# Performance work log

Hardware: AMD Instinct MI355X
Metric: run time of the kernel (lower is better)

Reference implementation:

```python
import jax, jax.numpy as jnp
import numpy as np

S, M, V, E, H = 128, 256, 32000, 1024, 512
PAD_ID = V - 1  # pad_id=-1 normalized to vocab-1


def setup_inputs() -> dict:
    key = jax.random.key(0)
    ks = jax.random.split(key, 9)
    F_lens = jax.random.randint(ks[0], (M,), 1, S + 1)
    tok = jax.random.randint(ks[1], (S, M), 1, PAD_ID)  # avoid 0 and PAD for valid tokens
    valid = jnp.arange(S)[:, None] < F_lens[None, :]
    F = jnp.where(valid, tok, PAD_ID)
    sc = 1.0 / np.sqrt(H)
    emb = jax.random.normal(ks[2], (V, E), jnp.float32) * 0.02
    emb = emb.at[PAD_ID].set(0.0)
    # PyTorch LSTM layout: gates [i, f, g, o]; bias_ih + bias_hh folded into one b.
    Wih0 = jax.random.uniform(ks[3], (2, 4 * H, E), jnp.float32, -sc, sc)
    Whh0 = jax.random.uniform(ks[4], (2, 4 * H, H), jnp.float32, -sc, sc)
    b0 = jax.random.uniform(ks[5], (2, 4 * H), jnp.float32, -sc, sc)
    Wih1 = jax.random.uniform(ks[6], (2, 4 * H, 2 * H), jnp.float32, -sc, sc)
    Whh1 = jax.random.uniform(ks[7], (2, 4 * H, H), jnp.float32, -sc, sc)
    b1 = jax.random.uniform(ks[8], (2, 4 * H), jnp.float32, -sc, sc)
    return dict(F=F, F_lens=F_lens, emb=emb, Wih0=Wih0, Whh0=Whh0, b0=b0,
                Wih1=Wih1, Whh1=Whh1, b1=b1)


def _run_lstm(x, mask, Wih, Whh, b):
    # x: [S, M, D], mask: [S, M] bool (update state only where valid, as packed seq does)
    m_ = x.shape[1]
    h_dim = Whh.shape[1]

    def step(carry, inp):
        h, c = carry
        xt, mt = inp
        g = xt @ Wih.T + h @ Whh.T + b
        i, f, gg, o = jnp.split(g, 4, axis=-1)
        c2 = jax.nn.sigmoid(f) * c + jax.nn.sigmoid(i) * jnp.tanh(gg)
        h2 = jax.nn.sigmoid(o) * jnp.tanh(c2)
        mt = mt[:, None]
        h2 = jnp.where(mt, h2, h)
        c2 = jnp.where(mt, c2, c)
        return (h2, c2), h2

    init = (jnp.zeros((m_, h_dim), x.dtype), jnp.zeros((m_, h_dim), x.dtype))
    _, hs = jax.lax.scan(step, init, (x, mask))
    return hs


def _bilstm_layer(x, mask, idx, Wih, Whh, b):
    # forward direction
    hf = _run_lstm(x, mask, Wih[0], Whh[0], b[0])
    # backward direction: per-sequence reverse within valid length (packed semantics)
    xr = jnp.take_along_axis(x, idx[:, :, None], axis=0)
    hb = _run_lstm(xr, mask, Wih[1], Whh[1], b[1])
    hb = jnp.take_along_axis(hb, idx[:, :, None], axis=0)  # idx is an involution on valid t
    return jnp.concatenate([hf, hb], axis=-1)


def reference(F, F_lens, emb, Wih0, Whh0, b0, Wih1, Whh1, b1):
    s_ = F.shape[0]
    t = jnp.arange(s_)[:, None]
    valid = t < F_lens[None, :]                      # [S, M]
    idx = jnp.where(valid, F_lens[None, :] - 1 - t, t)
    # embedding with padding_idx zeroing (matches nn.Embedding padding_idx + explicit loop)
    x = jnp.where((F != PAD_ID)[:, :, None], emb[F], 0.0)
    h1 = _bilstm_layer(x, valid, idx, Wih0, Whh0, b0)
    h2 = _bilstm_layer(h1, valid, idx, Wih1, Whh1, b1)
    # pad_packed_sequence(padding_value=h_pad=0) + final F==0 masking loop, fused
    keep = valid & (F != 0)
    return jnp.where(keep[:, :, None], h2, 0.0)
```

## Files before the change

### kernel.cpp

```cpp
#include <hip/hip_runtime.h>
#include <hip/hip_bf16.h>

#define S_LEN 128
#define M_B   256
#define E_DIM 1024
#define H_DIM 512
#define G4    2048
#define N_ROWS (S_LEN*M_B)
#define KD    1024

typedef __bf16 bf16_t;
typedef __bf16 bf16x8 __attribute__((ext_vector_type(8)));
typedef float  f32x4  __attribute__((ext_vector_type(4)));
typedef int    i32x4  __attribute__((ext_vector_type(4)));

#define AS1(p) ((const __attribute__((address_space(1))) void*)(p))
#define AS3(p) ((__attribute__((address_space(3))) void*)(p))

__device__ __forceinline__ float sigm(float x)     { return 1.f / (1.f + __expf(-x)); }
__device__ __forceinline__ float tanhfast(float x) { return 2.f / (1.f + __expf(-2.f * x)) - 1.f; }

__device__ __forceinline__ void store_h_dev(bf16_t* p, bf16_t v) {
    unsigned int w = (unsigned int)__builtin_bit_cast(unsigned short, v);
    asm volatile("global_store_short %0, %1, off sc0 sc1" :: "v"(p), "v"(w) : "memory");
}
__device__ __forceinline__ bf16x8 load_h_dev(const bf16_t* p) {
    i32x4 r;
    asm volatile("global_load_dwordx4 %0, %1, off sc0 sc1" : "=v"(r) : "v"(p) : "memory");
    return __builtin_bit_cast(bf16x8, r);
}
__device__ __forceinline__ f32x4 load_pv4(const float* p) {
    f32x4 r;
    asm volatile("global_load_dwordx4 %0, %1, off" : "=v"(r) : "v"(p) : "memory");
    return r;
}

__global__ __launch_bounds__(256)
void permute_all_kernel(const float* __restrict__ Wih0, const float* __restrict__ Whh0,
                        const float* __restrict__ b0,
                        const float* __restrict__ Wih1, const float* __restrict__ Whh1,
                        const float* __restrict__ b1,
                        bf16_t* __restrict__ Wih0p, bf16_t* __restrict__ Whh0p,
                        bf16_t* __restrict__ Wih1p, bf16_t* __restrict__ Whh1p,
                        float* __restrict__ b0p, float* __restrict__ b1p)
{
    int bid = blockIdx.x;
    int lay = bid >> 12;
    int d   = (bid >> 11) & 1;
    int jp  = bid & 2047;
    int q = jp >> 6, r = jp & 63;
    int gate = r >> 4, u16 = r & 15;
    int j = gate * H_DIM + q * 16 + u16;

    const float* Wih = lay ? Wih1 : Wih0;
    const float* Whh = lay ? Whh1 : Whh0;
    const float* b   = lay ? b1 : b0;
    bf16_t* Wihp = lay ? Wih1p : Wih0p;
    bf16_t* Whhp = lay ? Whh1p : Whh0p;
    float*  bp   = lay ? b1p : b0p;

    const float* s_ih = Wih + ((size_t)d * G4 + j) * E_DIM;
    bf16_t*      d_ih = Wihp + ((size_t)d * G4 + jp) * E_DIM;
    for (int e = threadIdx.x; e < E_DIM; e += 256) d_ih[e] = (bf16_t)s_ih[e];

    const float* s_hh = Whh + ((size_t)d * G4 + j) * H_DIM;
    bf16_t*      d_hh = Whhp + ((size_t)d * G4 + jp) * H_DIM;
    for (int k = threadIdx.x; k < H_DIM; k += 256) d_hh[k] = (bf16_t)s_hh[k];

    if (threadIdx.x == 0) bp[d * G4 + jp] = b[d * G4 + j];
}

__global__ __launch_bounds__(256)
void embed_kernel(const int* __restrict__ F, const float* __restrict__ emb,
                  const int* __restrict__ F_lens,
                  bf16_t* __restrict__ X, int* __restrict__ srcrow)
{
    int n   = blockIdx.x;
    int tok = F[n];
    const float4* src = (const float4*)(emb + (size_t)tok * E_DIM);
    bf16_t*       dst = X + (size_t)n * E_DIM;
    for (int i = threadIdx.x; i < E_DIM / 4; i += 256) {
        float4 v = src[i];
        dst[i * 4 + 0] = (bf16_t)v.x;
        dst[i * 4 + 1] = (bf16_t)v.y;
        dst[i * 4 + 2] = (bf16_t)v.z;
        dst[i * 4 + 3] = (bf16_t)v.w;
    }
    if (threadIdx.x == 0) {
        int t = n >> 8, m = n & 255;
        int L = F_lens[m];
        int st = (t < L) ? (L - 1 - t) : t;
        srcrow[n] = st * M_B + m;
    }
}

#define BM 128
#define BN 128
#define BKG 64

__global__ __launch_bounds__(256)
void gemm_pre_kernel(const bf16_t* __restrict__ A,
                     const bf16_t* __restrict__ Wp,
                     const float* __restrict__ bp,
                     const int* __restrict__ srcrow,
                     float* __restrict__ PREc,
                     int rowbase, int TCR)
{
    const int nwg = gridDim.x;
    const int qx  = nwg >> 3;
    const int orig = blockIdx.x;
    const int wg   = (orig & 7) * qx + (orig >> 3);
    const int MT   = TCR / BM;
    const int n_t  = wg & 15;
    const int m_t  = (wg >> 4) % MT;
    const int d    = wg / (16 * MT);

    const int n0   = n_t * BN;
    const int mloc = m_t * BM;
    const int tid  = threadIdx.x;
    const int lane = tid & 63, wave = tid >> 6;
    const int wm = wave >> 1, wn = wave & 1;
    const int fr = lane & 15, fq = lane >> 4;

    __shared__ __attribute__((aligned(16))) bf16_t At[BM * BKG];
    __shared__ __attribute__((aligned(16))) bf16_t Bt[BN * BKG];

    const int rA = tid >> 3;
    const int co = (((tid & 7) ^ (rA & 7)) << 3);
    size_t srowA[4];
    const bf16_t* Bp[4];
#pragma unroll
    for (int it = 0; it < 4; ++it) {
        int nn = rowbase + mloc + rA + it * 32;
        srowA[it] = (d == 1) ? (size_t)srcrow[nn] : (size_t)nn;
        Bp[it] = Wp + ((size_t)d * G4 + n0 + rA + it * 32) * KD + co;
    }

    f32x4 acc[4][4];
#pragma unroll
    for (int i = 0; i < 4; ++i)
#pragma unroll
        for (int j = 0; j < 4; ++j) { f32x4 z = {0.f, 0.f, 0.f, 0.f}; acc[i][j] = z; }

    for (int kt = 0; kt < KD; kt += BKG) {
#pragma unroll
        for (int it = 0; it < 4; ++it)
            __builtin_amdgcn_global_load_lds(AS1(A + srowA[it] * KD + kt + co),
                                             AS3(&At[(it * 256 + wave * 64) * 8]), 16, 0, 0);
#pragma unroll
        for (int it = 0; it < 4; ++it)
            __builtin_amdgcn_global_load_lds(AS1(Bp[it] + kt),
                                             AS3(&Bt[(it * 256 + wave * 64) * 8]), 16, 0, 0);
        __syncthreads();

        bf16x8 af[2][4], bff[2][4];
#pragma unroll
        for (int ks = 0; ks < 2; ++ks) {
#pragma unroll
            for (int i = 0; i < 4; ++i) {
                int ra = wm * 64 + i * 16 + fr;
                int ca = (ks * 4 + fq) ^ (ra & 7);
                af[ks][i] = *(const bf16x8*)&At[ra * BKG + ca * 8];
                int rb = wn * 64 + i * 16 + fr;
                int cbk = (ks * 4 + fq) ^ (rb & 7);
                bff[ks][i] = *(const bf16x8*)&Bt[rb * BKG + cbk * 8];
            }
        }
#pragma unroll
        for (int ks = 0; ks < 2; ++ks)
#pragma unroll
            for (int i = 0; i < 4; ++i)
#pragma unroll
                for (int j = 0; j < 4; ++j)
                    acc[i][j] = __builtin_amdgcn_mfma_f32_16x16x32_bf16(af[ks][i], bff[ks][j], acc[i][j], 0, 0, 0);
        __syncthreads();
    }

    const int ucol = ((n0 >> 6) + wn) * 16 + fr;
    float bq[4];
#pragma unroll
    for (int g = 0; g < 4; ++g) bq[g] = bp[d * G4 + n0 + wn * 64 + fr + g * 16];
#pragma unroll
    for (int mi = 0; mi < 4; ++mi) {
#pragma unroll
        for (int rr = 0; rr < 4; ++rr) {
            int r = mloc + wm * 64 + mi * 16 + fq * 4 + rr;
            f32x4 v;
#pragma unroll
            for (int g = 0; g < 4; ++g) v[g] = acc[mi][g][rr] + bq[g];
            *(f32x4*)&PREc[(((size_t)d * TCR + r) * 512 + ucol) * 4] = v;
        }
    }
}

__global__ __launch_bounds__(256)
void lstm_chunk_kernel(const bf16_t* __restrict__ Whhp,
                       const float* __restrict__ PREc,
                       const int* __restrict__ F_lens,
                       float* __restrict__ cfb,
                       bf16_t* __restrict__ hbA,
                       bf16_t* __restrict__ hbB,
                       bf16_t* __restrict__ H1,
                       float* __restrict__ OUT,
                       unsigned int* __restrict__ ctr,
                       int t0, int TC, int TCR, int mode, int s_base)
{
    const int d  = blockIdx.z;
    const int bx = blockIdx.x;
    const int m0 = blockIdx.y * 64;
    const int tid = threadIdx.x;
    const int lane = tid & 63, wave = tid >> 6;
    const int fr = lane & 15, fq = lane >> 4;
    const int gslot = ((blockIdx.y << 1) | d) * 16;

    __shared__ __attribute__((aligned(16))) bf16_t Bt[64 * 512];

    const bf16_t* Bg = Whhp + ((size_t)d * G4 + bx * 64) * H_DIM;
#pragma unroll
    for (int it = 0; it < 16; ++it) {
        int c   = it * 256 + tid;
        int row = c >> 6, ck = c & 63;
        int cks = ck ^ (row & 7);
        __builtin_amdgcn_global_load_lds(AS1(Bg + (size_t)row * H_DIM + cks * 8),
                                         AS3(&Bt[(it * 256 + wave * 64) * 8]), 16, 0, 0);
    }

    const int mrow  = m0 + wave * 16 + fr;
    const int u     = bx * 16 + fr;
    int mm[4], LL[4], sidx[4];
    float c_own[4], h_own[4];
    const float* pbase[4];
#pragma unroll
    for (int rr = 0; rr < 4; ++rr) {
        mm[rr]   = m0 + wave * 16 + fq * 4 + rr;
        LL[rr]   = F_lens[mm[rr]];
        sidx[rr] = (d * M_B + mm[rr]) * H_DIM + u;
        c_own[rr]= cfb[sidx[rr]];
        pbase[rr]= PREc + (((size_t)d * TCR + mm[rr]) * 512 + u) * 4;
    }
    {
        const bf16_t* hin0 = (t0 & 1) ? hbB : hbA;
#pragma unroll
        for (int rr = 0; rr < 4; ++rr) h_own[rr] = (float)hin0[sidx[rr]];
    }

    f32x4 pv[4];
#pragma unroll
    for (int rr = 0; rr < 4; ++rr)
        pv[rr] = load_pv4(pbase[rr]);

    __syncthreads();

    for (int tt = 0; tt < TC; ++tt) {
        const int t = t0 + tt;
        const bf16_t* hin  = (t & 1) ? hbB : hbA;
        bf16_t*       hout = (t & 1) ? hbA : hbB;

        const bf16_t* Arow = hin + ((size_t)d * M_B + mrow) * H_DIM + fq * 8;
        bf16x8 af[16];
#pragma unroll
        for (int ks = 0; ks < 16; ++ks)
            af[ks] = load_h_dev(Arow + ks * 32);
        asm volatile("s_waitcnt vmcnt(0)" ::: "memory");
        __builtin_amdgcn_sched_barrier(0);

        f32x4 acc[4];
#pragma unroll
        for (int j = 0; j < 4; ++j) { f32x4 z = {0.f, 0.f, 0.f, 0.f}; acc[j] = z; }

#pragma unroll
        for (int ks = 0; ks < 16; ++ks) {
#pragma unroll
            for (int j = 0; j < 4; ++j) {
                int rb = j * 16 + fr;
                int ck = (ks * 4 + fq) ^ (rb & 7);
                bf16x8 bf = *(const bf16x8*)&Bt[rb * 512 + ck * 8];
                acc[j] = __builtin_amdgcn_mfma_f32_16x16x32_bf16(af[ks], bf, acc[j], 0, 0, 0);
            }
        }

#pragma unroll
        for (int rr = 0; rr < 4; ++rr) {
            bool mt = (t < LL[rr]);
            float gi = acc[0][rr] + pv[rr][0];
            float gf = acc[1][rr] + pv[rr][1];
            float gg = acc[2][rr] + pv[rr][2];
            float go = acc[3][rr] + pv[rr][3];
            float c2 = sigm(gf) * c_own[rr] + sigm(gi) * tanhfast(gg);
            float h2 = sigm(go) * tanhfast(c2);
            if (!mt) { c2 = c_own[rr]; h2 = h_own[rr]; }
            c_own[rr] = c2;
            h_own[rr] = h2;
            store_h_dev(&hout[sidx[rr]], (bf16_t)h2);
        }
        asm volatile("s_waitcnt vmcnt(0)" ::: "memory");
        __syncthreads();
        if (tid == 0)
            __hip_atomic_fetch_add(&ctr[gslot], 1u, __ATOMIC_RELAXED, __HIP_MEMORY_SCOPE_AGENT);

#pragma unroll
        for (int rr = 0; rr < 4; ++rr) {
            bool mt = (t < LL[rr]);
            int trow = (d == 0 || !mt) ? t : (LL[rr] - 1 - t);
            size_t orow = (size_t)trow * M_B + mm[rr];
            if (mode == 0) H1[orow * 1024 + d * H_DIM + u] = (bf16_t)h_own[rr];
            else           OUT[orow * 1024 + d * H_DIM + u] = mt ? h_own[rr] : 0.f;
        }
        f32x4 pvn[4];
        if (tt + 1 < TC) {
#pragma unroll
            for (int rr = 0; rr < 4; ++rr)
                pvn[rr] = load_pv4(pbase[rr] + (size_t)(tt + 1) * ((size_t)M_B * G4));
        }

        if (tid == 0) {
            unsigned int tgt = (unsigned int)(s_base + tt + 1) * 32u;
            while (__hip_atomic_load(&ctr[gslot], __ATOMIC_RELAXED, __HIP_MEMORY_SCOPE_AGENT) < tgt)
                __builtin_amdgcn_s_sleep(2);
        }
        __syncthreads();

        if (tt + 1 < TC) {
#pragma unroll
            for (int rr = 0; rr < 4; ++rr)
                pv[rr] = pvn[rr];
        }
    }

#pragma unroll
    for (int rr = 0; rr < 4; ++rr) cfb[sidx[rr]] = c_own[rr];
}

extern "C" void kernel_launch(void* const* d_in, const int* in_sizes, int n_in,
                              void* d_out, int out_size, void* d_ws, size_t ws_size,
                              hipStream_t stream)
{
    const int*   F      = (const int*)d_in[0];
    const int*   F_lens = (const int*)d_in[1];
    const float* emb    = (const float*)d_in[2];
    const float* Wih0   = (const float*)d_in[3];
    const float* Whh0   = (const float*)d_in[4];
    const float* b0     = (const float*)d_in[5];
    const float* Wih1   = (const float*)d_in[6];
    const float* Whh1   = (const float*)d_in[7];
    const float* b1     = (const float*)d_in[8];
    float* OUT = (float*)d_out;

    char* p = (char*)d_ws;
    auto alloc = [&](size_t bytes) { char* q = p; p += (bytes + 255) & ~(size_t)255; return (void*)q; };
    bf16_t* X0    = (bf16_t*)alloc((size_t)N_ROWS * E_DIM * 2);
    bf16_t* H1    = (bf16_t*)alloc((size_t)N_ROWS * 1024 * 2);
    bf16_t* Wih0p = (bf16_t*)alloc((size_t)2 * G4 * E_DIM * 2);
    bf16_t* Whh0p = (bf16_t*)alloc((size_t)2 * G4 * H_DIM * 2);
    bf16_t* Wih1p = (bf16_t*)alloc((size_t)2 * G4 * E_DIM * 2);
    bf16_t* Whh1p = (bf16_t*)alloc((size_t)2 * G4 * H_DIM * 2);
    float*  b0p   = (float*)alloc((size_t)2 * G4 * 4);
    float*  b1p   = (float*)alloc((size_t)2 * G4 * 4);
    int*    srcrow= (int*)alloc((size_t)N_ROWS * 4);
    bf16_t* hbA   = (bf16_t*)alloc((size_t)2 * M_B * H_DIM * 2);
    bf16_t* hbB   = (bf16_t*)alloc((size_t)2 * M_B * H_DIM * 2);
    float*  cfb   = (float*)alloc((size_t)2 * M_B * H_DIM * 4);
    unsigned int* ctr = (unsigned int*)alloc(512);
    size_t base_used = (size_t)(p - (char*)d_ws);

    int TC = 0;
    const int tcs[8] = {128, 64, 32, 16, 8, 4, 2, 1};
    for (int i = 0; i < 8; ++i) {
        size_t need = base_used + (size_t)2 * tcs[i] * M_B * G4 * 4;
        if (need <= ws_size) { TC = tcs[i]; break; }
    }
    if (TC == 0) return;
    float* PREc = (float*)p;
    const int TCR = TC * M_B;

    hipMemsetAsync(ctr, 0, 512, stream);
    permute_all_kernel<<<dim3(2 * 2 * G4), 256, 0, stream>>>(
        Wih0, Whh0, b0, Wih1, Whh1, b1, Wih0p, Whh0p, Wih1p, Whh1p, b0p, b1p);
    embed_kernel<<<dim3(N_ROWS), 256, 0, stream>>>(F, emb, F_lens, X0, srcrow);

    for (int layer = 0; layer < 2; ++layer) {
        const bf16_t* Xin  = layer ? H1 : X0;
        const bf16_t* Wihp = layer ? Wih1p : Wih0p;
        const bf16_t* Whhp = layer ? Whh1p : Whh0p;
        const float*  bp   = layer ? b1p : b0p;

        hipMemsetAsync(hbA, 0, (size_t)2 * M_B * H_DIM * 2, stream);
        hipMemsetAsync(cfb, 0, (size_t)2 * M_B * H_DIM * 4, stream);

        for (int c = 0; c < S_LEN / TC; ++c) {
            gemm_pre_kernel<<<dim3(2 * (TCR / BM) * 16), 256, 0, stream>>>(
                Xin, Wihp, bp, srcrow, PREc, c * TCR, TCR);

            lstm_chunk_kernel<<<dim3(32, 4, 2), dim3(256), 0, stream>>>(
                Whhp, PREc, F_lens, cfb, hbA, hbB, H1, OUT, ctr,
                c * TC, TC, TCR, layer, layer * S_LEN + c * TC);
        }
    }
}
```

Baseline: 2.479 ms.

## Replace block-wide atomic counter barrier with per-wave flag array barrier

Swaps the per-timestep cross-block barrier, which used __syncthreads, a single atomic counter per group and a polling thread, for per-wave flag slots. Each wave publishes its step index with a coherent store, then polls all 32 peer blocks' flags in parallel using one lane per flag and a ballot. This removes the intra-block __syncthreads and the contention on a shared atomic, so waves can proceed independently. In exchange each wave issues more polling loads, and correctness depends on each wave only needing data written by the matching waves of other blocks.

```diff
diff --git a/kernel.cpp b/kernel.cpp
--- a/kernel.cpp
+++ b/kernel.cpp
@@ -32,6 +32,15 @@
 __device__ __forceinline__ f32x4 load_pv4(const float* p) {
     f32x4 r;
     asm volatile("global_load_dwordx4 %0, %1, off" : "=v"(r) : "v"(p) : "memory");
+    return r;
+}
+__device__ __forceinline__ void store_flag(unsigned int* p, unsigned int v) {
+    asm volatile("global_store_dword %0, %1, off sc0 sc1" :: "v"(p), "v"(v) : "memory");
+}
+__device__ __forceinline__ unsigned int load_flag(const unsigned int* p) {
+    unsigned int r;
+    asm volatile("global_load_dword %0, %1, off sc0 sc1\n\ts_waitcnt vmcnt(0)"
+                 : "=v"(r) : "v"(p) : "memory");
     return r;
 }
 
@@ -202,7 +211,7 @@
                        bf16_t* __restrict__ hbB,
                        bf16_t* __restrict__ H1,
                        float* __restrict__ OUT,
-                       unsigned int* __restrict__ ctr,
+                       unsigned int* __restrict__ flags,
                        int t0, int TC, int TCR, int mode, int s_base)
 {
     const int d  = blockIdx.z;
@@ -211,7 +220,7 @@
     const int tid = threadIdx.x;
     const int lane = tid & 63, wave = tid >> 6;
     const int fr = lane & 15, fq = lane >> 4;
-    const int gslot = ((blockIdx.y << 1) | d) * 16;
+    unsigned int* gflags = flags + ((((blockIdx.y << 1) | d) << 2) + wave) * 32;
 
     __shared__ __attribute__((aligned(16))) bf16_t Bt[64 * 512];
 
@@ -294,9 +303,8 @@
             store_h_dev(&hout[sidx[rr]], (bf16_t)h2);
         }
         asm volatile("s_waitcnt vmcnt(0)" ::: "memory");
-        __syncthreads();
-        if (tid == 0)
-            __hip_atomic_fetch_add(&ctr[gslot], 1u, __ATOMIC_RELAXED, __HIP_MEMORY_SCOPE_AGENT);
+        if (lane == 0)
+            store_flag(&gflags[bx], (unsigned int)(s_base + tt + 1));
 
 #pragma unroll
         for (int rr = 0; rr < 4; ++rr) {
@@ -313,12 +321,12 @@
                 pvn[rr] = load_pv4(pbase[rr] + (size_t)(tt + 1) * ((size_t)M_B * G4));
         }
 
-        if (tid == 0) {
-            unsigned int tgt = (unsigned int)(s_base + tt + 1) * 32u;
-            while (__hip_atomic_load(&ctr[gslot], __ATOMIC_RELAXED, __HIP_MEMORY_SCOPE_AGENT) < tgt)
-                __builtin_amdgcn_s_sleep(2);
-        }
-        __syncthreads();
+        {
+            const unsigned int tgt = (unsigned int)(s_base + tt + 1);
+            const unsigned int* fp = &gflags[lane & 31];
+            while (__ballot(load_flag(fp) >= tgt) != ~0ull)
+                __builtin_amdgcn_s_sleep(1);
+        }
 
         if (tt + 1 < TC) {
 #pragma unroll
@@ -360,7 +368,7 @@
     bf16_t* hbA   = (bf16_t*)alloc((size_t)2 * M_B * H_DIM * 2);
     bf16_t* hbB   = (bf16_t*)alloc((size_t)2 * M_B * H_DIM * 2);
     float*  cfb   = (float*)alloc((size_t)2 * M_B * H_DIM * 4);
-    unsigned int* ctr = (unsigned int*)alloc(512);
+    unsigned int* flags = (unsigned int*)alloc(4096);
     size_t base_used = (size_t)(p - (char*)d_ws);
 
     int TC = 0;
@@ -373,7 +381,7 @@
     float* PREc = (float*)p;
     const int TCR = TC * M_B;
 
-    hipMemsetAsync(ctr, 0, 512, stream);
+    hipMemsetAsync(flags, 0, 4096, stream);
     permute_all_kernel<<<dim3(2 * 2 * G4), 256, 0, stream>>>(
         Wih0, Whh0, b0, Wih1, Whh1, b1, Wih0p, Whh0p, Wih1p, Whh1p, b0p, b1p);
     embed_kernel<<<dim3(N_ROWS), 256, 0, stream>>>(F, emb, F_lens, X0, srcrow);
@@ -392,7 +400,7 @@
                 Xin, Wihp, bp, srcrow, PREc, c * TCR, TCR);
 
             lstm_chunk_kernel<<<dim3(32, 4, 2), dim3(256), 0, stream>>>(
-                Whhp, PREc, F_lens, cfb, hbA, hbB, H1, OUT, ctr,
+                Whhp, PREc, F_lens, cfb, hbA, hbB, H1, OUT, flags,
                 c * TC, TC, TCR, layer, layer * S_LEN + c * TC);
         }
     }
```

Result: faster. 2.401 ms (-3.1%).
